# Optimization experiments

Measured on AMD Instinct MI355X. Metric: run time of the kernel, lower is better.

## Reference

```python
import jax, jax.numpy as jnp
import numpy as np

V = 200000      # num_symbols
E = 128         # embed_dim
PAD = V - 1     # padding index
KNN_K = 32
BQ, BS, NN, KT = 2048, 5, 128, 64
D = 2 * E       # d_model
STEPS = 4
H = 2 * D       # LSTMCell hidden


def setup_inputs():
    key = jax.random.key(0)
    ks = jax.random.split(key, 20)
    f = lambda k, s: jax.random.normal(k, s, dtype=jnp.float32) * 0.02
    emb = f(ks[0], (V, E)).at[PAD].set(0.0)  # padding row is zeros
    return dict(
        emb=emb,
        gcn_W=f(ks[1], (E, D)), gcn_wb=jnp.zeros((E,), jnp.float32),
        gate_W=f(ks[2], (1, D)), gate_b=jnp.zeros((1,), jnp.float32),
        se_w1=f(ks[3], (2 * D, D)), se_b1=jnp.zeros((2 * D,), jnp.float32),
        se_w2=f(ks[4], (D, 2 * D)), se_b2=jnp.zeros((D,), jnp.float32),
        ln_g=jnp.ones((D,), jnp.float32), ln_b=jnp.zeros((D,), jnp.float32),
        W_ih=f(ks[5], (4 * H, D)), W_hh=f(ks[6], (4 * H, H)),
        b_ih=jnp.zeros((4 * H,), jnp.float32), b_hh=jnp.zeros((4 * H,), jnp.float32),
        query=jax.random.randint(ks[7], (BQ, 2), 0, V),
        support=jax.random.randint(ks[8], (BS, 2), 0, V),
        q_l_conn=jax.random.randint(ks[9], (BQ, NN, 2), 0, V),
        q_l_deg=jax.random.randint(ks[10], (BQ,), 1, NN),
        q_r_conn=jax.random.randint(ks[11], (BQ, NN, 2), 0, V),
        q_r_deg=jax.random.randint(ks[12], (BQ,), 1, NN),
        s_l_conn=jax.random.randint(ks[13], (BS, NN, 2), 0, V),
        s_l_deg=jax.random.randint(ks[14], (BS,), 1, NN),
        s_r_conn=jax.random.randint(ks[15], (BS, NN, 2), 0, V),
        s_r_deg=jax.random.randint(ks[16], (BS,), 1, NN),
        knn_tab=jax.random.randint(ks[17], (V, KT), 0, V),
    )


def _cos(a, b):
    # F.cosine_similarity with eps=1e-8
    eps = 1e-8
    na = jnp.maximum(jnp.linalg.norm(a, axis=-1), eps)
    nb = jnp.maximum(jnp.linalg.norm(b, axis=-1), eps)
    return jnp.sum(a * b, axis=-1) / (na * nb)


def _neighbor_encoder(conn, eids, emb, gcn_W, gcn_wb, gate_W, gate_b, knn_tab):
    eids = jnp.where((eids < 0) | (eids >= V), PAD, eids)
    rel_e = emb[conn[..., 0]]            # [B,N,E]
    ent_e = emb[conn[..., 1]]            # [B,N,E]
    center = emb[eids][:, None, :]       # [B,1,E]
    # cosine-sim top-k neighbor selection
    sim = _cos(center, ent_e)            # [B,N]
    _, idx = jax.lax.top_k(sim, KNN_K)
    rel_k = jnp.take_along_axis(rel_e, idx[..., None], axis=1)
    ent_k = jnp.take_along_axis(ent_e, idx[..., None], axis=1)
    cat = jnp.concatenate([rel_k, ent_k], axis=-1)         # [B,k,2E]
    structural = jnp.tanh(jnp.mean(cat @ gcn_W.T + gcn_wb, axis=1))  # [B,E]
    # KNN-index branch
    kidx = knn_tab[eids]
    kidx = jnp.where((kidx < 0) | (kidx >= V), PAD, kidx)
    knn_e = emb[kidx]                    # [B,KT,E]
    sim2 = _cos(center, knn_e)
    _, idx2 = jax.lax.top_k(sim2, KNN_K)
    knn_k_e = jnp.take_along_axis(knn_e, idx2[..., None], axis=1)
    pad_rel = jnp.broadcast_to(emb[PAD], knn_k_e.shape)    # pad relation embedding
    cat2 = jnp.concatenate([pad_rel, knn_k_e], axis=-1)
    knn_mean = jnp.tanh(jnp.mean(cat2 @ gcn_W.T + gcn_wb, axis=1))
    # sigmoid gate fusing structural + knn representation
    gate_in = jnp.concatenate([structural, knn_mean], axis=-1)
    alpha = jax.nn.sigmoid(gate_in @ gate_W.T + gate_b)    # [B,1]
    return (1.0 - alpha) * structural + alpha * knn_mean


def _support_enc(x, w1, b1, w2, b2, g, b):
    h = jax.nn.relu(x @ w1.T + b1) @ w2.T + b2 + x
    mu = jnp.mean(h, axis=-1, keepdims=True)
    var = jnp.var(h, axis=-1, keepdims=True)
    return (h - mu) / jnp.sqrt(var + 1e-5) * g + b


def _query_enc(support, query, W_ih, W_hh, b_ih, b_hh):
    # GMatching LSTMCell matching network; support: [1,D], query: [B,D]
    B = query.shape[0]

    def step(carry, _):
        h_r, c = carry
        z = query @ W_ih.T + b_ih + h_r @ W_hh.T + b_hh
        i, f, g, o = jnp.split(z, 4, axis=-1)
        c2 = jax.nn.sigmoid(f) * c + jax.nn.sigmoid(i) * jnp.tanh(g)
        h2 = jax.nn.sigmoid(o) * jnp.tanh(c2)
        h = query + h2[:, :D]
        attn = jax.nn.softmax(h @ support.T, axis=1)       # [B,1]
        r = attn @ support                                  # [B,D]
        return (jnp.concatenate([h, r], axis=1), c2), h

    z0 = jnp.zeros((B, H), query.dtype)
    _, hs = jax.lax.scan(step, (z0, z0), None, length=STEPS)
    return hs[-1]


def reference(emb, gcn_W, gcn_wb, gate_W, gate_b, se_w1, se_b1, se_w2, se_b2,
              ln_g, ln_b, W_ih, W_hh, b_ih, b_hh,
              query, support, q_l_conn, q_l_deg, q_r_conn, q_r_deg,
              s_l_conn, s_l_deg, s_r_conn, s_r_deg, knn_tab):
    ne = lambda conn, eids: _neighbor_encoder(conn, eids, emb, gcn_W, gcn_wb,
                                              gate_W, gate_b, knn_tab)
    ql = ne(q_l_conn, query[:, 0])
    qr = ne(q_r_conn, query[:, 1])
    sl = ne(s_l_conn, support[:, 0])
    sr = ne(s_r_conn, support[:, 1])
    query_n = jnp.concatenate([ql, qr], axis=-1)   # [BQ,D]
    supp_n = jnp.concatenate([sl, sr], axis=-1)    # [BS,D]
    se = lambda x: _support_enc(x, se_w1, se_b1, se_w2, se_b2, ln_g, ln_b)
    support_g = jnp.mean(se(supp_n), axis=0, keepdims=True)   # [1,D]
    query_g = se(query_n)                                      # [BQ,D]
    query_f = _query_enc(support_g, query_g, W_ih, W_hh, b_ih, b_hh)
    qf = query_f / jnp.maximum(jnp.linalg.norm(query_f, axis=-1, keepdims=True), 1e-12)
    sg = support_g / jnp.maximum(jnp.linalg.norm(support_g, axis=-1, keepdims=True), 1e-12)
    return (qf @ sg.T).squeeze(-1)   # [BQ]
```

## Files before the change

### kernel.cpp

```cpp
#include <hip/hip_runtime.h>

#define Vn 200000
#define PADI 199999

typedef unsigned short ushort_t;
typedef unsigned int uint_t;
typedef __attribute__((ext_vector_type(8))) short short8;
typedef __attribute__((ext_vector_type(4))) float float4v;

__device__ __forceinline__ float sigm(float x) { return 1.f / (1.f + expf(-x)); }
__device__ __forceinline__ float dot4(float4 a, float4 b) {
  return a.x*b.x + a.y*b.y + a.z*b.z + a.w*b.w;
}
__device__ __forceinline__ ushort_t f2bf(float x) {
  uint_t u = __float_as_uint(x);
  uint_t r = (u + 0x7fffu + ((u >> 16) & 1u)) >> 16;
  return (ushort_t)r;
}
__device__ __forceinline__ float bf2f(ushort_t h) { return __uint_as_float(((uint_t)h) << 16); }

__device__ __forceinline__ float2 block_reduce2(float a, float b, float2* red) {
  #pragma unroll
  for (int off = 32; off; off >>= 1) { a += __shfl_down(a, off); b += __shfl_down(b, off); }
  __syncthreads();
  if ((threadIdx.x & 63) == 0) red[threadIdx.x >> 6] = make_float2(a, b);
  __syncthreads();
  float2 r;
  r.x = red[0].x + red[1].x + red[2].x + red[3].x;
  r.y = red[0].y + red[1].y + red[2].y + red[3].y;
  return r;
}

__global__ __launch_bounds__(256) void transpose_kernel(
    const float* __restrict__ in, float* __restrict__ out, int R, int Cfull, int c0, int Ct) {
  int idx = blockIdx.x * 256 + threadIdx.x;
  if (idx >= R * Ct) return;
  int c = idx / R, r = idx - c * R;
  out[idx] = in[(size_t)r * Cfull + c0 + c];
}

__global__ __launch_bounds__(256) void build_b2t_kernel(
    const float* __restrict__ W, ushort_t* __restrict__ b2t, int strideK) {
  int n = blockIdx.x, k = threadIdx.x;
  float v = W[(size_t)n*strideK + k];
  ushort_t hi = f2bf(v);
  ushort_t lo = f2bf(v - bf2f(hi));
  ushort_t* row = b2t + (size_t)n*768;
  row[k] = hi; row[256 + k] = hi; row[512 + k] = lo;
}

__global__ __launch_bounds__(256) void bias_sum_kernel(
    const float* __restrict__ a, const float* __restrict__ b, float* __restrict__ o) {
  int i = blockIdx.x*256 + threadIdx.x;
  o[i] = a[i] + b[i];
}

__global__ __launch_bounds__(256) void gemm_bf16_kernel(
    const ushort_t* __restrict__ A2, const ushort_t* __restrict__ B2T,
    float* __restrict__ C, const float* __restrict__ addmat,
    const float* __restrict__ cv, int ldc) {
  __shared__ ushort_t As[128*40];
  __shared__ ushort_t Bs[128*40];
  int t = threadIdx.x;
  int m0 = blockIdx.y * 128, n0 = blockIdx.x * 128;
  int wid = t >> 6, lane = t & 63;
  int wm = (wid >> 1) * 64, wn = (wid & 1) * 64;
  int q = lane >> 4, fr = lane & 15;
  float4v acc[4][4];
  #pragma unroll
  for (int i = 0; i < 4; ++i)
    #pragma unroll
    for (int j = 0; j < 4; ++j) acc[i][j] = (float4v)0.f;

  for (int k0 = 0; k0 < 768; k0 += 32) {
    #pragma unroll
    for (int rnd = 0; rnd < 2; ++rnd) {
      int idx = rnd*256 + t;
      int row = idx >> 2, ch = idx & 3;
      *(short8*)&As[row*40 + ch*8] = *(const short8*)(A2 + (size_t)(m0+row)*768 + k0 + ch*8);
      *(short8*)&Bs[row*40 + ch*8] = *(const short8*)(B2T + (size_t)(n0+row)*768 + k0 + ch*8);
    }
    __syncthreads();
    short8 af[4], bg[4];
    #pragma unroll
    for (int tm = 0; tm < 4; ++tm) af[tm] = *(const short8*)&As[(wm + tm*16 + fr)*40 + q*8];
    #pragma unroll
    for (int tn = 0; tn < 4; ++tn) bg[tn] = *(const short8*)&Bs[(wn + tn*16 + fr)*40 + q*8];
    #pragma unroll
    for (int tm = 0; tm < 4; ++tm)
      #pragma unroll
      for (int tn = 0; tn < 4; ++tn)
        acc[tm][tn] = __builtin_amdgcn_mfma_f32_16x16x32_bf16(af[tm], bg[tn], acc[tm][tn], 0, 0, 0);
    __syncthreads();
  }

  #pragma unroll
  for (int tm = 0; tm < 4; ++tm) {
    int gm = m0 + wm + tm*16 + q*4;
    #pragma unroll
    for (int tn = 0; tn < 4; ++tn) {
      int gn = n0 + wn + tn*16 + fr;
      float cvv = cv ? cv[gn] : 0.f;
      #pragma unroll
      for (int reg = 0; reg < 4; ++reg) {
        size_t off = (size_t)(gm + reg) * ldc + gn;
        float x = acc[tm][tn][reg] + cvv;
        if (addmat) x += addmat[off];
        C[off] = x;
      }
    }
  }
}

__global__ __launch_bounds__(256) void enc_kernel(
    const float* __restrict__ emb, const float* __restrict__ gcnW, const float* __restrict__ gcnb,
    const float* __restrict__ gateW, const float* __restrict__ gateb,
    const int* __restrict__ knn_tab,
    const int* __restrict__ query, const int* __restrict__ support,
    const int* __restrict__ qlc, const int* __restrict__ qrc,
    const int* __restrict__ slc, const int* __restrict__ src,
    float* __restrict__ xbuf) {
  __shared__ float center[128];
  __shared__ float sims[128];
  __shared__ float sims2[64];
  __shared__ int idr[128], ide[128];
  __shared__ int kidxs[64];
  __shared__ int sel[32], sel2[32];
  __shared__ int cnt1, cnt2;
  __shared__ float catbuf[256];
  __shared__ float knnA[128], knnB[128];
  __shared__ float part1[256], part2[256];
  __shared__ float structural[128], knnm[128];
  __shared__ float2 red2[4];

  int t = threadIdx.x;
  int g = blockIdx.x;
  int eid; const int* conn; float* outp;
  if (g < 2048)      { eid = query[2*g];                 conn = qlc + (size_t)g*256;      outp = xbuf + (size_t)g*256; }
  else if (g < 4096) { int b = g-2048; eid = query[2*b+1];  conn = qrc + (size_t)b*256;   outp = xbuf + (size_t)b*256 + 128; }
  else if (g < 4101) { int b = g-4096; eid = support[2*b];  conn = slc + (size_t)b*256;   outp = xbuf + (size_t)(2048+b)*256; }
  else               { int b = g-4101; eid = support[2*b+1]; conn = src + (size_t)b*256;  outp = xbuf + (size_t)(2048+b)*256 + 128; }
  if (eid < 0 || eid >= Vn) eid = PADI;

  if (t == 0) { cnt1 = 0; cnt2 = 0; }
  if (t < 128) {
    int2 cc = ((const int2*)conn)[t];
    idr[t] = cc.x; ide[t] = cc.y;
    center[t] = emb[(size_t)eid*128 + t];
  } else if (t < 192) {
    int kk = knn_tab[(size_t)eid*64 + (t-128)];
    kidxs[t-128] = (kk < 0 || kk >= Vn) ? PADI : kk;
  }
  __syncthreads();

  int gid = t >> 4, ll = t & 15;
  float4 cen0 = *(const float4*)&center[ll*8];
  float4 cen1 = *(const float4*)&center[ll*8 + 4];
  float cn2 = dot4(cen0, cen0) + dot4(cen1, cen1);
  #pragma unroll
  for (int off = 8; off; off >>= 1) cn2 += __shfl_down(cn2, off, 16);
  cn2 = __shfl(cn2, 0, 16);
  float cn = fmaxf(sqrtf(cn2), 1e-8f);

  #pragma unroll 2
  for (int it = 0; it < 4; ++it) {
    int n0 = it*32 + gid*2;
    int e0 = ide[n0], e1 = ide[n0+1];
    const float4* p0 = (const float4*)(emb + (size_t)e0*128);
    const float4* p1 = (const float4*)(emb + (size_t)e1*128);
    float4 a0 = p0[ll*2], b0 = p0[ll*2+1];
    float4 a1 = p1[ll*2], b1 = p1[ll*2+1];
    float d0 = dot4(a0, cen0) + dot4(b0, cen1), m0 = dot4(a0, a0) + dot4(b0, b0);
    float d1 = dot4(a1, cen0) + dot4(b1, cen1), m1 = dot4(a1, a1) + dot4(b1, b1);
    #pragma unroll
    for (int off = 8; off; off >>= 1) {
      d0 += __shfl_down(d0, off, 16); m0 += __shfl_down(m0, off, 16);
      d1 += __shfl_down(d1, off, 16); m1 += __shfl_down(m1, off, 16);
    }
    if (ll == 0) {
      sims[n0]   = d0 / (cn * fmaxf(sqrtf(m0), 1e-8f));
      sims[n0+1] = d1 / (cn * fmaxf(sqrtf(m1), 1e-8f));
    }
  }
  #pragma unroll 2
  for (int it = 0; it < 2; ++it) {
    int n0 = it*32 + gid*2;
    int e0 = kidxs[n0], e1 = kidxs[n0+1];
    const float4* p0 = (const float4*)(emb + (size_t)e0*128);
    const float4* p1 = (const float4*)(emb + (size_t)e1*128);
    float4 a0 = p0[ll*2], b0 = p0[ll*2+1];
    float4 a1 = p1[ll*2], b1 = p1[ll*2+1];
    float d0 = dot4(a0, cen0) + dot4(b0, cen1), m0 = dot4(a0, a0) + dot4(b0, b0);
    float d1 = dot4(a1, cen0) + dot4(b1, cen1), m1 = dot4(a1, a1) + dot4(b1, b1);
    #pragma unroll
    for (int off = 8; off; off >>= 1) {
      d0 += __shfl_down(d0, off, 16); m0 += __shfl_down(m0, off, 16);
      d1 += __shfl_down(d1, off, 16); m1 += __shfl_down(m1, off, 16);
    }
    if (ll == 0) {
      sims2[n0]   = d0 / (cn * fmaxf(sqrtf(m0), 1e-8f));
      sims2[n0+1] = d1 / (cn * fmaxf(sqrtf(m1), 1e-8f));
    }
  }
  __syncthreads();

  if (t < 128) {
    float my = sims[t];
    int c = 0;
    for (int j = 0; j < 128; ++j) {
      float sj = sims[j];
      c += (sj > my) || (sj == my && j < t);
    }
    if (c < 32) { int p = atomicAdd(&cnt1, 1); sel[p] = t; }
  } else if (t < 192) {
    int i = t - 128;
    float my = sims2[i];
    int c = 0;
    for (int j = 0; j < 64; ++j) {
      float sj = sims2[j];
      c += (sj > my) || (sj == my && j < i);
    }
    if (c < 32) { int p = atomicAdd(&cnt2, 1); sel2[p] = i; }
  }
  __syncthreads();

  {
    int i = t & 127;
    float a0 = 0.f, a1 = 0.f, a2 = 0.f, a3 = 0.f;
    float k0 = 0.f, k1 = 0.f;
    if (t < 128) {
      #pragma unroll 2
      for (int k = 0; k < 32; k += 4) {
        a0 += emb[(size_t)idr[sel[k+0]]*128 + i];
        a1 += emb[(size_t)idr[sel[k+1]]*128 + i];
        a2 += emb[(size_t)idr[sel[k+2]]*128 + i];
        a3 += emb[(size_t)idr[sel[k+3]]*128 + i];
      }
      catbuf[i] = (a0+a1+a2+a3) * (1.f/32.f);
      #pragma unroll 2
      for (int k = 0; k < 16; k += 2) {
        k0 += emb[(size_t)kidxs[sel2[k+0]]*128 + i];
        k1 += emb[(size_t)kidxs[sel2[k+1]]*128 + i];
      }
      knnA[i] = k0 + k1;
    } else {
      #pragma unroll 2
      for (int k = 0; k < 32; k += 4) {
        a0 += emb[(size_t)ide[sel[k+0]]*128 + i];
        a1 += emb[(size_t)ide[sel[k+1]]*128 + i];
        a2 += emb[(size_t)ide[sel[k+2]]*128 + i];
        a3 += emb[(size_t)ide[sel[k+3]]*128 + i];
      }
      catbuf[128 + i] = (a0+a1+a2+a3) * (1.f/32.f);
      #pragma unroll 2
      for (int k = 16; k < 32; k += 2) {
        k0 += emb[(size_t)kidxs[sel2[k+0]]*128 + i];
        k1 += emb[(size_t)kidxs[sel2[k+1]]*128 + i];
      }
      knnB[i] = k0 + k1;
    }
  }
  __syncthreads();

  {
    int i = t & 127, half = t >> 7;
    const float4* w1p = (const float4*)(gcnW + (size_t)i*256 + half*128);
    const float4* c1p = (const float4*)(catbuf + half*128);
    float p1 = 0.f;
    #pragma unroll 8
    for (int j = 0; j < 32; ++j) {
      float4 w = w1p[j], a = c1p[j];
      p1 += dot4(w, a);
    }
    const float4* w2p = (const float4*)(gcnW + (size_t)i*256 + 128 + half*64);
    const float4* kap = (const float4*)(knnA + half*64);
    const float4* kbp = (const float4*)(knnB + half*64);
    float p2 = 0.f;
    #pragma unroll 8
    for (int j = 0; j < 16; ++j) {
      float4 w = w2p[j], xa = kap[j], xb = kbp[j];
      float4 s = make_float4(xa.x+xb.x, xa.y+xb.y, xa.z+xb.z, xa.w+xb.w);
      p2 += dot4(w, s);
    }
    part1[t] = p1;
    part2[t] = p2 * (1.f/32.f);
  }
  __syncthreads();
  if (t < 128) {
    structural[t] = tanhf(part1[t] + part1[t+128] + gcnb[t]);
    knnm[t]       = tanhf(part2[t] + part2[t+128] + gcnb[t]);
  }
  __syncthreads();

  float gv = (t < 128) ? structural[t]*gateW[t] : knnm[t-128]*gateW[t];
  float2 rr = block_reduce2(gv, 0.f, red2);
  float alpha = sigm(rr.x + gateb[0]);
  if (t < 128) outp[t] = (1.f - alpha)*structural[t] + alpha*knnm[t];
}

__global__ __launch_bounds__(256) void qenc_kernel(
    const float* __restrict__ xin, const float* __restrict__ w1t, const float* __restrict__ b1,
    const float* __restrict__ w2t, const float* __restrict__ b2,
    const float* __restrict__ lng, const float* __restrict__ lnb,
    float* __restrict__ xout, ushort_t* __restrict__ a2) {
  __shared__ float xs[8][256];
  __shared__ float hsm[8][512];
  __shared__ float2 red2[4];
  int t = threadIdx.x;
  int r0 = blockIdx.x * 8;
  #pragma unroll
  for (int rr = 0; rr < 8; ++rr) xs[rr][t] = xin[(size_t)(r0+rr)*256 + t];
  __syncthreads();
  #pragma unroll
  for (int uo = 0; uo < 512; uo += 256) {
    int u = uo + t;
    float bv = b1[u];
    float acc[8];
    #pragma unroll
    for (int rr = 0; rr < 8; ++rr) acc[rr] = bv;
    for (int j4 = 0; j4 < 64; ++j4) {
      float w0 = w1t[(size_t)(j4*4+0)*512 + u];
      float w1v = w1t[(size_t)(j4*4+1)*512 + u];
      float w2v = w1t[(size_t)(j4*4+2)*512 + u];
      float w3 = w1t[(size_t)(j4*4+3)*512 + u];
      #pragma unroll
      for (int rr = 0; rr < 8; ++rr) {
        float4 x = *(const float4*)&xs[rr][j4*4];
        acc[rr] += x.x*w0 + x.y*w1v + x.z*w2v + x.w*w3;
      }
    }
    #pragma unroll
    for (int rr = 0; rr < 8; ++rr) hsm[rr][u] = fmaxf(acc[rr], 0.f);
  }
  __syncthreads();
  float val[8];
  {
    float bv = b2[t];
    #pragma unroll
    for (int rr = 0; rr < 8; ++rr) val[rr] = bv + xs[rr][t];
    for (int u4 = 0; u4 < 128; ++u4) {
      float w0 = w2t[(size_t)(u4*4+0)*256 + t];
      float w1v = w2t[(size_t)(u4*4+1)*256 + t];
      float w2v = w2t[(size_t)(u4*4+2)*256 + t];
      float w3 = w2t[(size_t)(u4*4+3)*256 + t];
      #pragma unroll
      for (int rr = 0; rr < 8; ++rr) {
        float4 h4 = *(const float4*)&hsm[rr][u4*4];
        val[rr] += h4.x*w0 + h4.y*w1v + h4.z*w2v + h4.w*w3;
      }
    }
  }
  float gv = lng[t], bv2 = lnb[t];
  for (int rr = 0; rr < 8; ++rr) {
    int r = r0 + rr;
    float2 sq = block_reduce2(val[rr], val[rr]*val[rr], red2);
    float mu  = sq.x * (1.f/256.f);
    float var = sq.y * (1.f/256.f) - mu*mu;
    float rs  = 1.f / sqrtf(var + 1e-5f);
    float ov  = (val[rr] - mu) * rs * gv + bv2;
    xout[(size_t)r*256 + t] = ov;
    if (r < 2048) {
      ushort_t hi = f2bf(ov);
      ushort_t lo = f2bf(ov - bf2f(hi));
      ushort_t* row = a2 + (size_t)r*768;
      row[t] = hi; row[256 + t] = lo; row[512 + t] = hi;
    }
  }
}

__global__ __launch_bounds__(256) void finalize_kernel(
    const float* __restrict__ qout, const float* __restrict__ whh,
    float* __restrict__ sg_hat, float* __restrict__ z_supp) {
  __shared__ float sg[256];
  __shared__ float2 red2[4];
  int t = threadIdx.x;
  float acc = 0.f;
  #pragma unroll
  for (int s = 0; s < 5; ++s) acc += qout[(size_t)(2048+s)*256 + t];
  float sgv = acc * 0.2f;
  sg[t] = sgv;
  float2 nn = block_reduce2(sgv*sgv, 0.f, red2);
  if (blockIdx.x == 0) sg_hat[t] = sgv / fmaxf(sqrtf(nn.x), 1e-12f);
  __syncthreads();
  int u = blockIdx.x*256 + t;
  const float4* w4 = (const float4*)(whh + (size_t)u*512 + 256);
  float a = 0.f;
  #pragma unroll 4
  for (int j4 = 0; j4 < 64; ++j4) {
    float4 wv = w4[j4];
    float4 sv = *(const float4*)&sg[j4*4];
    a += dot4(wv, sv);
  }
  z_supp[u] = a;
}

__global__ __launch_bounds__(256) void gate_kernel(
    const float* __restrict__ Z, const float* __restrict__ qg,
    float* __restrict__ c, ushort_t* __restrict__ a2, int step0) {
  int idx = blockIdx.x * 256 + threadIdx.x;
  int r = idx >> 9, j = idx & 511;
  const float* zr = Z + (size_t)r * 1792;
  float zi = zr[j], zf = zr[512 + j], zg = zr[1024 + j];
  float cold = step0 ? 0.f : c[idx];
  float c2 = sigm(zf) * cold + sigm(zi) * tanhf(zg);
  c[idx] = c2;
  if (j < 256) {
    float zo = zr[1536 + j];
    float h = qg[(size_t)r*256 + j] + sigm(zo) * tanhf(c2);
    ushort_t hi = f2bf(h);
    ushort_t lo = f2bf(h - bf2f(hi));
    ushort_t* row = a2 + (size_t)r*768;
    row[j] = hi; row[256 + j] = lo; row[512 + j] = hi;
  }
}

__global__ __launch_bounds__(256) void gatecos_kernel(
    const float* __restrict__ Z, const float* __restrict__ qg, const float* __restrict__ c,
    const float* __restrict__ sgh, float* __restrict__ out) {
  int wid = threadIdx.x >> 6, lane = threadIdx.x & 63;
  int r = blockIdx.x*4 + wid;
  const float* zr = Z + (size_t)r * 1792;
  float d = 0.f, n2 = 0.f;
  #pragma unroll
  for (int i = 0; i < 4; ++i) {
    int j = lane + i*64;
    float zi = zr[j], zf = zr[512 + j], zg = zr[1024 + j], zo = zr[1536 + j];
    float cold = c[(size_t)r*512 + j];
    float c2 = sigm(zf) * cold + sigm(zi) * tanhf(zg);
    float h = qg[(size_t)r*256 + j] + sigm(zo) * tanhf(c2);
    d += h * sgh[j];
    n2 += h * h;
  }
  #pragma unroll
  for (int off = 32; off; off >>= 1) { d += __shfl_down(d, off); n2 += __shfl_down(n2, off); }
  if (lane == 0) out[r] = d / fmaxf(sqrtf(n2), 1e-12f);
}

extern "C" void kernel_launch(void* const* d_in, const int* in_sizes, int n_in,
                              void* d_out, int out_size, void* d_ws, size_t ws_size,
                              hipStream_t stream) {
  const float* emb   = (const float*)d_in[0];
  const float* gcnW  = (const float*)d_in[1];
  const float* gcnb  = (const float*)d_in[2];
  const float* gateW = (const float*)d_in[3];
  const float* gateb = (const float*)d_in[4];
  const float* sew1  = (const float*)d_in[5];
  const float* seb1  = (const float*)d_in[6];
  const float* sew2  = (const float*)d_in[7];
  const float* seb2  = (const float*)d_in[8];
  const float* lng   = (const float*)d_in[9];
  const float* lnb   = (const float*)d_in[10];
  const float* Wih   = (const float*)d_in[11];
  const float* Whh   = (const float*)d_in[12];
  const float* bih   = (const float*)d_in[13];
  const float* bhh   = (const float*)d_in[14];
  const int* query   = (const int*)d_in[15];
  const int* support = (const int*)d_in[16];
  const int* qlc     = (const int*)d_in[17];
  const int* qrc     = (const int*)d_in[19];
  const int* slc     = (const int*)d_in[21];
  const int* src     = (const int*)d_in[23];
  const int* knn     = (const int*)d_in[25];
  float* out = (float*)d_out;

  float* w = (float*)d_ws;
  size_t o = 0;
  auto alloc = [&](size_t n) { float* p = w + o; o += (n + 15) & ~(size_t)15; return p; };
  float* xbuf      = alloc((size_t)2056*256);
  float* query_g   = alloc((size_t)2056*256);
  float* sg_hat    = alloc(256);
  float* z_supp    = alloc(1792);
  float* cbuf      = alloc((size_t)2048*512);
  float* Abuf      = alloc((size_t)2048*1792);
  float* Zbuf      = alloc((size_t)2048*1792);
  float* w1t       = alloc(256*512);
  float* w2t       = alloc(512*256);
  float* bias_s    = alloc(1792);
  ushort_t* A2     = (ushort_t*)alloc((size_t)2048*768/2);
  ushort_t* B2ih   = (ushort_t*)alloc((size_t)1792*768/2);
  ushort_t* B2hh   = (ushort_t*)alloc((size_t)1792*768/2);
  (void)ws_size; (void)in_sizes; (void)n_in; (void)out_size;

  transpose_kernel<<<512,  256, 0, stream>>>(sew1, w1t, 512, 256, 0, 256);
  transpose_kernel<<<1024, 256, 0, stream>>>(sew2, w2t, 256, 512, 0, 512);
  build_b2t_kernel<<<1792, 256, 0, stream>>>(Wih, B2ih, 256);
  build_b2t_kernel<<<1792, 256, 0, stream>>>(Whh, B2hh, 512);
  bias_sum_kernel<<<7, 256, 0, stream>>>(bih, bhh, bias_s);

  enc_kernel<<<4106, 256, 0, stream>>>(emb, gcnW, gcnb, gateW, gateb, knn,
                                       query, support, qlc, qrc, slc, src, xbuf);

  qenc_kernel<<<257, 256, 0, stream>>>(xbuf, w1t, seb1, w2t, seb2, lng, lnb, query_g, A2);

  finalize_kernel<<<7, 256, 0, stream>>>(query_g, Whh, sg_hat, z_supp);

  gemm_bf16_kernel<<<dim3(14,16), 256, 0, stream>>>(A2, B2ih, Abuf, nullptr, bias_s, 1792);
  gate_kernel<<<4096, 256, 0, stream>>>(Abuf, query_g, cbuf, A2, 1);
  for (int s = 1; s < 4; ++s) {
    gemm_bf16_kernel<<<dim3(14,16), 256, 0, stream>>>(A2, B2hh, Zbuf, Abuf, z_supp, 1792);
    if (s < 3) gate_kernel<<<4096, 256, 0, stream>>>(Zbuf, query_g, cbuf, A2, 0);
    else       gatecos_kernel<<<512, 256, 0, stream>>>(Zbuf, query_g, cbuf, sg_hat, out);
  }
}
```

Baseline: 581.8 us.

## Fuse LSTM pipeline into one persistent kernel with grid barriers

Merges the query-encoder, finalize, four GEMMs and gate kernels into a single persistent kernel of 448 blocks synchronized by atomic grid barriers. The five weight-prep kernels are merged into one launch, and the encoder's two similarity loops are unified into one pass that handles four rows at a time. The GEMM tile shrinks to 128x64 so the grid covers more blocks. The aim is to remove launch overhead and tail gaps between the many small kernels. In exchange it relies on all blocks being co-resident for the spin barrier, and the smaller GEMM tiles reuse less data.

Measured after the change: 998.9 us. 1.72x slower.

```diff
diff --git a/kernel.cpp b/kernel.cpp
--- a/kernel.cpp
+++ b/kernel.cpp
@@ -2,6 +2,7 @@
 
 #define Vn 200000
 #define PADI 199999
+#define NBLK 448
 
 typedef unsigned short ushort_t;
 typedef unsigned int uint_t;
@@ -31,84 +32,53 @@
   return r;
 }
 
-__global__ __launch_bounds__(256) void transpose_kernel(
-    const float* __restrict__ in, float* __restrict__ out, int R, int Cfull, int c0, int Ct) {
-  int idx = blockIdx.x * 256 + threadIdx.x;
-  if (idx >= R * Ct) return;
-  int c = idx / R, r = idx - c * R;
-  out[idx] = in[(size_t)r * Cfull + c0 + c];
-}
-
-__global__ __launch_bounds__(256) void build_b2t_kernel(
-    const float* __restrict__ W, ushort_t* __restrict__ b2t, int strideK) {
-  int n = blockIdx.x, k = threadIdx.x;
-  float v = W[(size_t)n*strideK + k];
-  ushort_t hi = f2bf(v);
-  ushort_t lo = f2bf(v - bf2f(hi));
-  ushort_t* row = b2t + (size_t)n*768;
-  row[k] = hi; row[256 + k] = hi; row[512 + k] = lo;
-}
-
-__global__ __launch_bounds__(256) void bias_sum_kernel(
-    const float* __restrict__ a, const float* __restrict__ b, float* __restrict__ o) {
-  int i = blockIdx.x*256 + threadIdx.x;
-  o[i] = a[i] + b[i];
-}
-
-__global__ __launch_bounds__(256) void gemm_bf16_kernel(
-    const ushort_t* __restrict__ A2, const ushort_t* __restrict__ B2T,
-    float* __restrict__ C, const float* __restrict__ addmat,
-    const float* __restrict__ cv, int ldc) {
-  __shared__ ushort_t As[128*40];
-  __shared__ ushort_t Bs[128*40];
-  int t = threadIdx.x;
-  int m0 = blockIdx.y * 128, n0 = blockIdx.x * 128;
-  int wid = t >> 6, lane = t & 63;
-  int wm = (wid >> 1) * 64, wn = (wid & 1) * 64;
-  int q = lane >> 4, fr = lane & 15;
-  float4v acc[4][4];
-  #pragma unroll
-  for (int i = 0; i < 4; ++i)
-    #pragma unroll
-    for (int j = 0; j < 4; ++j) acc[i][j] = (float4v)0.f;
-
-  for (int k0 = 0; k0 < 768; k0 += 32) {
-    #pragma unroll
-    for (int rnd = 0; rnd < 2; ++rnd) {
-      int idx = rnd*256 + t;
-      int row = idx >> 2, ch = idx & 3;
-      *(short8*)&As[row*40 + ch*8] = *(const short8*)(A2 + (size_t)(m0+row)*768 + k0 + ch*8);
-      *(short8*)&Bs[row*40 + ch*8] = *(const short8*)(B2T + (size_t)(n0+row)*768 + k0 + ch*8);
-    }
-    __syncthreads();
-    short8 af[4], bg[4];
-    #pragma unroll
-    for (int tm = 0; tm < 4; ++tm) af[tm] = *(const short8*)&As[(wm + tm*16 + fr)*40 + q*8];
-    #pragma unroll
-    for (int tn = 0; tn < 4; ++tn) bg[tn] = *(const short8*)&Bs[(wn + tn*16 + fr)*40 + q*8];
-    #pragma unroll
-    for (int tm = 0; tm < 4; ++tm)
-      #pragma unroll
-      for (int tn = 0; tn < 4; ++tn)
-        acc[tm][tn] = __builtin_amdgcn_mfma_f32_16x16x32_bf16(af[tm], bg[tn], acc[tm][tn], 0, 0, 0);
-    __syncthreads();
-  }
-
-  #pragma unroll
-  for (int tm = 0; tm < 4; ++tm) {
-    int gm = m0 + wm + tm*16 + q*4;
-    #pragma unroll
-    for (int tn = 0; tn < 4; ++tn) {
-      int gn = n0 + wn + tn*16 + fr;
-      float cvv = cv ? cv[gn] : 0.f;
-      #pragma unroll
-      for (int reg = 0; reg < 4; ++reg) {
-        size_t off = (size_t)(gm + reg) * ldc + gn;
-        float x = acc[tm][tn][reg] + cvv;
-        if (addmat) x += addmat[off];
-        C[off] = x;
-      }
-    }
+__device__ __forceinline__ void grid_bar(unsigned* cnt, int& phase) {
+  __syncthreads();
+  if (threadIdx.x == 0) {
+    phase++;
+    __threadfence();
+    __hip_atomic_fetch_add(cnt, 1u, __ATOMIC_RELEASE, __HIP_MEMORY_SCOPE_AGENT);
+    while (__hip_atomic_load(cnt, __ATOMIC_RELAXED, __HIP_MEMORY_SCOPE_AGENT) <
+           (unsigned)(NBLK * phase))
+      __builtin_amdgcn_s_sleep(2);
+    __threadfence();
+  }
+  __syncthreads();
+}
+
+__global__ __launch_bounds__(256) void prep_kernel(
+    const float* __restrict__ sew1, const float* __restrict__ sew2,
+    const float* __restrict__ Wih, const float* __restrict__ Whh,
+    const float* __restrict__ bih, const float* __restrict__ bhh,
+    float* __restrict__ w1t, float* __restrict__ w2t,
+    ushort_t* __restrict__ B2ih, ushort_t* __restrict__ B2hh,
+    float* __restrict__ bias_s, unsigned* __restrict__ bar) {
+  int b = blockIdx.x, t = threadIdx.x;
+  if (b < 512) {
+    int idx = b*256 + t;
+    int c = idx >> 9, r = idx & 511;
+    w1t[idx] = sew1[(size_t)r*256 + c];
+  } else if (b < 1024) {
+    int idx = (b-512)*256 + t;
+    int c = idx >> 8, r = idx & 255;
+    w2t[idx] = sew2[(size_t)r*512 + c];
+  } else if (b < 2816) {
+    int n = b - 1024;
+    float v = Wih[(size_t)n*256 + t];
+    ushort_t hi = f2bf(v), lo = f2bf(v - bf2f(hi));
+    ushort_t* row = B2ih + (size_t)n*768;
+    row[t] = hi; row[256+t] = hi; row[512+t] = lo;
+  } else if (b < 4608) {
+    int n = b - 2816;
+    float v = Whh[(size_t)n*512 + t];
+    ushort_t hi = f2bf(v), lo = f2bf(v - bf2f(hi));
+    ushort_t* row = B2hh + (size_t)n*768;
+    row[t] = hi; row[256+t] = hi; row[512+t] = lo;
+  } else if (b < 4615) {
+    int i = (b-4608)*256 + t;
+    bias_s[i] = bih[i] + bhh[i];
+  } else {
+    if (t < 8) bar[t] = 0u;
   }
 }
 
@@ -121,8 +91,7 @@
     const int* __restrict__ slc, const int* __restrict__ src,
     float* __restrict__ xbuf) {
   __shared__ float center[128];
-  __shared__ float sims[128];
-  __shared__ float sims2[64];
+  __shared__ float simsu[192];
   __shared__ int idr[128], ide[128];
   __shared__ int kidxs[64];
   __shared__ int sel[32], sel2[32];
@@ -162,62 +131,53 @@
   cn2 = __shfl(cn2, 0, 16);
   float cn = fmaxf(sqrtf(cn2), 1e-8f);
 
-  #pragma unroll 2
-  for (int it = 0; it < 4; ++it) {
-    int n0 = it*32 + gid*2;
-    int e0 = ide[n0], e1 = ide[n0+1];
-    const float4* p0 = (const float4*)(emb + (size_t)e0*128);
-    const float4* p1 = (const float4*)(emb + (size_t)e1*128);
-    float4 a0 = p0[ll*2], b0 = p0[ll*2+1];
-    float4 a1 = p1[ll*2], b1 = p1[ll*2+1];
-    float d0 = dot4(a0, cen0) + dot4(b0, cen1), m0 = dot4(a0, a0) + dot4(b0, b0);
-    float d1 = dot4(a1, cen0) + dot4(b1, cen1), m1 = dot4(a1, a1) + dot4(b1, b1);
+  #pragma unroll
+  for (int it = 0; it < 3; ++it) {
+    int rbase = it*64 + gid*4;
+    int e[4];
+    #pragma unroll
+    for (int rr = 0; rr < 4; ++rr) {
+      int n = rbase + rr;
+      e[rr] = (n < 128) ? ide[n] : kidxs[n-128];
+    }
+    float d[4], m[4];
+    #pragma unroll
+    for (int rr = 0; rr < 4; ++rr) {
+      const float4* p = (const float4*)(emb + (size_t)e[rr]*128);
+      float4 a = p[ll*2], bb = p[ll*2+1];
+      d[rr] = dot4(a, cen0) + dot4(bb, cen1);
+      m[rr] = dot4(a, a) + dot4(bb, bb);
+    }
     #pragma unroll
     for (int off = 8; off; off >>= 1) {
-      d0 += __shfl_down(d0, off, 16); m0 += __shfl_down(m0, off, 16);
-      d1 += __shfl_down(d1, off, 16); m1 += __shfl_down(m1, off, 16);
+      #pragma unroll
+      for (int rr = 0; rr < 4; ++rr) {
+        d[rr] += __shfl_down(d[rr], off, 16);
+        m[rr] += __shfl_down(m[rr], off, 16);
+      }
     }
     if (ll == 0) {
-      sims[n0]   = d0 / (cn * fmaxf(sqrtf(m0), 1e-8f));
-      sims[n0+1] = d1 / (cn * fmaxf(sqrtf(m1), 1e-8f));
-    }
-  }
-  #pragma unroll 2
-  for (int it = 0; it < 2; ++it) {
-    int n0 = it*32 + gid*2;
-    int e0 = kidxs[n0], e1 = kidxs[n0+1];
-    const float4* p0 = (const float4*)(emb + (size_t)e0*128);
-    const float4* p1 = (const float4*)(emb + (size_t)e1*128);
-    float4 a0 = p0[ll*2], b0 = p0[ll*2+1];
-    float4 a1 = p1[ll*2], b1 = p1[ll*2+1];
-    float d0 = dot4(a0, cen0) + dot4(b0, cen1), m0 = dot4(a0, a0) + dot4(b0, b0);
-    float d1 = dot4(a1, cen0) + dot4(b1, cen1), m1 = dot4(a1, a1) + dot4(b1, b1);
-    #pragma unroll
-    for (int off = 8; off; off >>= 1) {
-      d0 += __shfl_down(d0, off, 16); m0 += __shfl_down(m0, off, 16);
-      d1 += __shfl_down(d1, off, 16); m1 += __shfl_down(m1, off, 16);
-    }
-    if (ll == 0) {
-      sims2[n0]   = d0 / (cn * fmaxf(sqrtf(m0), 1e-8f));
-      sims2[n0+1] = d1 / (cn * fmaxf(sqrtf(m1), 1e-8f));
+      #pragma unroll
+      for (int rr = 0; rr < 4; ++rr)
+        simsu[rbase+rr] = d[rr] / (cn * fmaxf(sqrtf(m[rr]), 1e-8f));
     }
   }
   __syncthreads();
 
   if (t < 128) {
-    float my = sims[t];
+    float my = simsu[t];
     int c = 0;
     for (int j = 0; j < 128; ++j) {
-      float sj = sims[j];
+      float sj = simsu[j];
       c += (sj > my) || (sj == my && j < t);
     }
     if (c < 32) { int p = atomicAdd(&cnt1, 1); sel[p] = t; }
   } else if (t < 192) {
     int i = t - 128;
-    float my = sims2[i];
+    float my = simsu[128 + i];
     int c = 0;
     for (int j = 0; j < 64; ++j) {
-      float sj = sims2[j];
+      float sj = simsu[128 + j];
       c += (sj > my) || (sj == my && j < i);
     }
     if (c < 32) { int p = atomicAdd(&cnt2, 1); sel2[p] = i; }
@@ -298,142 +258,220 @@
   if (t < 128) outp[t] = (1.f - alpha)*structural[t] + alpha*knnm[t];
 }
 
-__global__ __launch_bounds__(256) void qenc_kernel(
-    const float* __restrict__ xin, const float* __restrict__ w1t, const float* __restrict__ b1,
+__device__ __forceinline__ void gemm_phase(
+    const ushort_t* __restrict__ A2, const ushort_t* __restrict__ B2T,
+    float* __restrict__ C, const float* __restrict__ addmat, const float* __restrict__ cv,
+    int bx, int by, int t, char* smem) {
+  ushort_t* As = (ushort_t*)smem;
+  ushort_t* Bs = (ushort_t*)(smem + 10240);
+  int m0 = by*128, n0 = bx*64;
+  int wid = t >> 6, lane = t & 63;
+  int wm = (wid >> 1) * 64, wn = (wid & 1) * 32;
+  int q = lane >> 4, fr = lane & 15;
+  float4v acc[4][2];
+  #pragma unroll
+  for (int i = 0; i < 4; ++i) { acc[i][0] = (float4v)0.f; acc[i][1] = (float4v)0.f; }
+
+  int row = t >> 2, ch = t & 3;
+  for (int k0 = 0; k0 < 768; k0 += 32) {
+    *(short8*)&As[row*40 + ch*8]      = *(const short8*)(A2 + (size_t)(m0+row)*768 + k0 + ch*8);
+    *(short8*)&As[(row+64)*40 + ch*8] = *(const short8*)(A2 + (size_t)(m0+row+64)*768 + k0 + ch*8);
+    *(short8*)&Bs[row*40 + ch*8]      = *(const short8*)(B2T + (size_t)(n0+row)*768 + k0 + ch*8);
+    __syncthreads();
+    short8 af[4], bg[2];
+    #pragma unroll
+    for (int mt = 0; mt < 4; ++mt) af[mt] = *(const short8*)&As[(wm + mt*16 + fr)*40 + q*8];
+    #pragma unroll
+    for (int nt = 0; nt < 2; ++nt) bg[nt] = *(const short8*)&Bs[(wn + nt*16 + fr)*40 + q*8];
+    #pragma unroll
+    for (int mt = 0; mt < 4; ++mt)
+      #pragma unroll
+      for (int nt = 0; nt < 2; ++nt)
+        acc[mt][nt] = __builtin_amdgcn_mfma_f32_16x16x32_bf16(af[mt], bg[nt], acc[mt][nt], 0, 0, 0);
+    __syncthreads();
+  }
+  #pragma unroll
+  for (int mt = 0; mt < 4; ++mt) {
+    int gm = m0 + wm + mt*16 + q*4;
+    #pragma unroll
+    for (int nt = 0; nt < 2; ++nt) {
+      int gn = n0 + wn + nt*16 + fr;
+      float cvv = cv ? cv[gn] : 0.f;
+      #pragma unroll
+      for (int reg = 0; reg < 4; ++reg) {
+        size_t off = (size_t)(gm + reg) * 1792 + gn;
+        float x = acc[mt][nt][reg] + cvv;
+        if (addmat) x += addmat[off];
+        C[off] = x;
+      }
+    }
+  }
+}
+
+__device__ __forceinline__ void gate_phase(
+    const float* __restrict__ Z, const float* __restrict__ qg,
+    float* __restrict__ c, ushort_t* __restrict__ a2, int step0, int b, int t) {
+  for (int idx = b*256 + t; idx < 2048*512; idx += NBLK*256) {
+    int r = idx >> 9, j = idx & 511;
+    const float* zr = Z + (size_t)r * 1792;
+    float zi = zr[j], zf = zr[512 + j], zg = zr[1024 + j];
+    float cold = step0 ? 0.f : c[idx];
+    float c2 = sigm(zf) * cold + sigm(zi) * tanhf(zg);
+    c[idx] = c2;
+    if (j < 256) {
+      float zo = zr[1536 + j];
+      float h = qg[(size_t)r*256 + j] + sigm(zo) * tanhf(c2);
+      ushort_t hi = f2bf(h), lo = f2bf(h - bf2f(hi));
+      ushort_t* row = a2 + (size_t)r*768;
+      row[j] = hi; row[256 + j] = lo; row[512 + j] = hi;
+    }
+  }
+}
+
+__global__ __launch_bounds__(256, 2) void lstm_kernel(
+    const float* __restrict__ xbuf, const float* __restrict__ w1t, const float* __restrict__ b1,
     const float* __restrict__ w2t, const float* __restrict__ b2,
     const float* __restrict__ lng, const float* __restrict__ lnb,
-    float* __restrict__ xout, ushort_t* __restrict__ a2) {
-  __shared__ float xs[8][256];
-  __shared__ float hsm[8][512];
-  __shared__ float2 red2[4];
+    const float* __restrict__ whh_full,
+    const ushort_t* __restrict__ B2ih, const ushort_t* __restrict__ B2hh,
+    const float* __restrict__ bias_s,
+    float* __restrict__ qg, ushort_t* __restrict__ A2,
+    float* __restrict__ z_supp, float* __restrict__ sg_hat,
+    float* __restrict__ Abuf, float* __restrict__ Zbuf, float* __restrict__ cbuf,
+    float* __restrict__ outv, unsigned* __restrict__ bar) {
+  __shared__ __align__(16) char smem[24640];
   int t = threadIdx.x;
-  int r0 = blockIdx.x * 8;
-  #pragma unroll
-  for (int rr = 0; rr < 8; ++rr) xs[rr][t] = xin[(size_t)(r0+rr)*256 + t];
-  __syncthreads();
-  #pragma unroll
-  for (int uo = 0; uo < 512; uo += 256) {
-    int u = uo + t;
-    float bv = b1[u];
-    float acc[8];
-    #pragma unroll
-    for (int rr = 0; rr < 8; ++rr) acc[rr] = bv;
+  int b = blockIdx.x;
+  int phase = 0;
+
+  if (b < 257) {
+    float (*xs)[256]  = (float (*)[256])smem;
+    float (*hsm)[512] = (float (*)[512])(smem + 8192);
+    float2* red2 = (float2*)(smem + 8192 + 16384);
+    int r0 = b * 8;
+    #pragma unroll
+    for (int rr = 0; rr < 8; ++rr) xs[rr][t] = xbuf[(size_t)(r0+rr)*256 + t];
+    __syncthreads();
+    #pragma unroll
+    for (int uo = 0; uo < 512; uo += 256) {
+      int u = uo + t;
+      float bv = b1[u];
+      float acc[8];
+      #pragma unroll
+      for (int rr = 0; rr < 8; ++rr) acc[rr] = bv;
+      for (int j4 = 0; j4 < 64; ++j4) {
+        float w0 = w1t[(size_t)(j4*4+0)*512 + u];
+        float w1v = w1t[(size_t)(j4*4+1)*512 + u];
+        float w2v = w1t[(size_t)(j4*4+2)*512 + u];
+        float w3 = w1t[(size_t)(j4*4+3)*512 + u];
+        #pragma unroll
+        for (int rr = 0; rr < 8; ++rr) {
+          float4 x = *(const float4*)&xs[rr][j4*4];
+          acc[rr] += x.x*w0 + x.y*w1v + x.z*w2v + x.w*w3;
+        }
+      }
+      #pragma unroll
+      for (int rr = 0; rr < 8; ++rr) hsm[rr][u] = fmaxf(acc[rr], 0.f);
+    }
+    __syncthreads();
+    float val[8];
+    {
+      float bv = b2[t];
+      #pragma unroll
+      for (int rr = 0; rr < 8; ++rr) val[rr] = bv + xs[rr][t];
+      for (int u4 = 0; u4 < 128; ++u4) {
+        float w0 = w2t[(size_t)(u4*4+0)*256 + t];
+        float w1v = w2t[(size_t)(u4*4+1)*256 + t];
+        float w2v = w2t[(size_t)(u4*4+2)*256 + t];
+        float w3 = w2t[(size_t)(u4*4+3)*256 + t];
+        #pragma unroll
+        for (int rr = 0; rr < 8; ++rr) {
+          float4 h4 = *(const float4*)&hsm[rr][u4*4];
+          val[rr] += h4.x*w0 + h4.y*w1v + h4.z*w2v + h4.w*w3;
+        }
+      }
+    }
+    float gvv = lng[t], bv2 = lnb[t];
+    for (int rr = 0; rr < 8; ++rr) {
+      int r = r0 + rr;
+      float2 sq = block_reduce2(val[rr], val[rr]*val[rr], red2);
+      float mu  = sq.x * (1.f/256.f);
+      float var = sq.y * (1.f/256.f) - mu*mu;
+      float rs  = 1.f / sqrtf(var + 1e-5f);
+      float ov  = (val[rr] - mu) * rs * gvv + bv2;
+      qg[(size_t)r*256 + t] = ov;
+      if (r < 2048) {
+        ushort_t hi = f2bf(ov), lo = f2bf(ov - bf2f(hi));
+        ushort_t* row = A2 + (size_t)r*768;
+        row[t] = hi; row[256 + t] = lo; row[512 + t] = hi;
+      }
+    }
+  }
+  grid_bar(bar, phase);
+
+  if (b < 7) {
+    float* sg = (float*)smem;
+    float2* red2 = (float2*)(smem + 1024);
+    float acc = 0.f;
+    #pragma unroll
+    for (int s = 0; s < 5; ++s) acc += qg[(size_t)(2048+s)*256 + t];
+    float sgv = acc * 0.2f;
+    sg[t] = sgv;
+    float2 nn = block_reduce2(sgv*sgv, 0.f, red2);
+    if (b == 0) sg_hat[t] = sgv / fmaxf(sqrtf(nn.x), 1e-12f);
+    __syncthreads();
+    int u = b*256 + t;
+    const float4* w4 = (const float4*)(whh_full + (size_t)u*512 + 256);
+    float a = 0.f;
+    #pragma unroll 4
     for (int j4 = 0; j4 < 64; ++j4) {
-      float w0 = w1t[(size_t)(j4*4+0)*512 + u];
-      float w1v = w1t[(size_t)(j4*4+1)*512 + u];
-      float w2v = w1t[(size_t)(j4*4+2)*512 + u];
-      float w3 = w1t[(size_t)(j4*4+3)*512 + u];
-      #pragma unroll
-      for (int rr = 0; rr < 8; ++rr) {
-        float4 x = *(const float4*)&xs[rr][j4*4];
-        acc[rr] += x.x*w0 + x.y*w1v + x.z*w2v + x.w*w3;
-      }
-    }
-    #pragma unroll
-    for (int rr = 0; rr < 8; ++rr) hsm[rr][u] = fmaxf(acc[rr], 0.f);
-  }
-  __syncthreads();
-  float val[8];
-  {
-    float bv = b2[t];
-    #pragma unroll
-    for (int rr = 0; rr < 8; ++rr) val[rr] = bv + xs[rr][t];
-    for (int u4 = 0; u4 < 128; ++u4) {
-      float w0 = w2t[(size_t)(u4*4+0)*256 + t];
-      float w1v = w2t[(size_t)(u4*4+1)*256 + t];
-      float w2v = w2t[(size_t)(u4*4+2)*256 + t];
-      float w3 = w2t[(size_t)(u4*4+3)*256 + t];
-      #pragma unroll
-      for (int rr = 0; rr < 8; ++rr) {
-        float4 h4 = *(const float4*)&hsm[rr][u4*4];
-        val[rr] += h4.x*w0 + h4.y*w1v + h4.z*w2v + h4.w*w3;
-      }
-    }
-  }
-  float gv = lng[t], bv2 = lnb[t];
-  for (int rr = 0; rr < 8; ++rr) {
-    int r = r0 + rr;
-    float2 sq = block_reduce2(val[rr], val[rr]*val[rr], red2);
-    float mu  = sq.x * (1.f/256.f);
-    float var = sq.y * (1.f/256.f) - mu*mu;
-    float rs  = 1.f / sqrtf(var + 1e-5f);
-    float ov  = (val[rr] - mu) * rs * gv + bv2;
-    xout[(size_t)r*256 + t] = ov;
-    if (r < 2048) {
-      ushort_t hi = f2bf(ov);
-      ushort_t lo = f2bf(ov - bf2f(hi));
-      ushort_t* row = a2 + (size_t)r*768;
-      row[t] = hi; row[256 + t] = lo; row[512 + t] = hi;
-    }
-  }
-}
-
-__global__ __launch_bounds__(256) void finalize_kernel(
-    const float* __restrict__ qout, const float* __restrict__ whh,
-    float* __restrict__ sg_hat, float* __restrict__ z_supp) {
-  __shared__ float sg[256];
-  __shared__ float2 red2[4];
-  int t = threadIdx.x;
-  float acc = 0.f;
-  #pragma unroll
-  for (int s = 0; s < 5; ++s) acc += qout[(size_t)(2048+s)*256 + t];
-  float sgv = acc * 0.2f;
-  sg[t] = sgv;
-  float2 nn = block_reduce2(sgv*sgv, 0.f, red2);
-  if (blockIdx.x == 0) sg_hat[t] = sgv / fmaxf(sqrtf(nn.x), 1e-12f);
-  __syncthreads();
-  int u = blockIdx.x*256 + t;
-  const float4* w4 = (const float4*)(whh + (size_t)u*512 + 256);
-  float a = 0.f;
-  #pragma unroll 4
-  for (int j4 = 0; j4 < 64; ++j4) {
-    float4 wv = w4[j4];
-    float4 sv = *(const float4*)&sg[j4*4];
-    a += dot4(wv, sv);
-  }
-  z_supp[u] = a;
-}
-
-__global__ __launch_bounds__(256) void gate_kernel(
-    const float* __restrict__ Z, const float* __restrict__ qg,
-    float* __restrict__ c, ushort_t* __restrict__ a2, int step0) {
-  int idx = blockIdx.x * 256 + threadIdx.x;
-  int r = idx >> 9, j = idx & 511;
-  const float* zr = Z + (size_t)r * 1792;
-  float zi = zr[j], zf = zr[512 + j], zg = zr[1024 + j];
-  float cold = step0 ? 0.f : c[idx];
-  float c2 = sigm(zf) * cold + sigm(zi) * tanhf(zg);
-  c[idx] = c2;
-  if (j < 256) {
-    float zo = zr[1536 + j];
-    float h = qg[(size_t)r*256 + j] + sigm(zo) * tanhf(c2);
-    ushort_t hi = f2bf(h);
-    ushort_t lo = f2bf(h - bf2f(hi));
-    ushort_t* row = a2 + (size_t)r*768;
-    row[j] = hi; row[256 + j] = lo; row[512 + j] = hi;
-  }
-}
-
-__global__ __launch_bounds__(256) void gatecos_kernel(
-    const float* __restrict__ Z, const float* __restrict__ qg, const float* __restrict__ c,
-    const float* __restrict__ sgh, float* __restrict__ out) {
-  int wid = threadIdx.x >> 6, lane = threadIdx.x & 63;
-  int r = blockIdx.x*4 + wid;
-  const float* zr = Z + (size_t)r * 1792;
-  float d = 0.f, n2 = 0.f;
-  #pragma unroll
-  for (int i = 0; i < 4; ++i) {
-    int j = lane + i*64;
-    float zi = zr[j], zf = zr[512 + j], zg = zr[1024 + j], zo = zr[1536 + j];
-    float cold = c[(size_t)r*512 + j];
-    float c2 = sigm(zf) * cold + sigm(zi) * tanhf(zg);
-    float h = qg[(size_t)r*256 + j] + sigm(zo) * tanhf(c2);
-    d += h * sgh[j];
-    n2 += h * h;
-  }
-  #pragma unroll
-  for (int off = 32; off; off >>= 1) { d += __shfl_down(d, off); n2 += __shfl_down(n2, off); }
-  if (lane == 0) out[r] = d / fmaxf(sqrtf(n2), 1e-12f);
+      float4 wv = w4[j4];
+      float4 sv = *(const float4*)&sg[j4*4];
+      a += dot4(wv, sv);
+    }
+    z_supp[u] = a;
+    __syncthreads();
+  }
+
+  gemm_phase(A2, B2ih, Abuf, nullptr, bias_s, b % 28, b / 28, t, smem);
+  grid_bar(bar, phase);
+
+  gate_phase(Abuf, qg, cbuf, A2, 1, b, t);
+  grid_bar(bar, phase);
+
+  for (int s = 1; s <= 3; ++s) {
+    if (s < 3) {
+      gemm_phase(A2, B2hh, Zbuf, Abuf, z_supp, b % 28, b / 28, t, smem);
+    } else if (b < 256) {
+      int bxi = b & 15, by = b >> 4;
+      int bx = (bxi >> 2) * 8 + (bxi & 3);
+      gemm_phase(A2, B2hh, Zbuf, Abuf, z_supp, bx, by, t, smem);
+    }
+    grid_bar(bar, phase);
+    if (s < 3) {
+      gate_phase(Zbuf, qg, cbuf, A2, 0, b, t);
+      grid_bar(bar, phase);
+    } else {
+      int wid = t >> 6, lane = t & 63;
+      for (int r = b*4 + wid; r < 2048; r += NBLK*4) {
+        const float* zr = Zbuf + (size_t)r * 1792;
+        float d = 0.f, n2 = 0.f;
+        #pragma unroll
+        for (int i = 0; i < 4; ++i) {
+          int j = lane + i*64;
+          float zi = zr[j], zf = zr[512 + j], zg = zr[1024 + j], zo = zr[1536 + j];
+          float cold = cbuf[(size_t)r*512 + j];
+          float c2 = sigm(zf) * cold + sigm(zi) * tanhf(zg);
+          float h = qg[(size_t)r*256 + j] + sigm(zo) * tanhf(c2);
+          d += h * sg_hat[j];
+          n2 += h * h;
+        }
+        #pragma unroll
+        for (int off = 32; off; off >>= 1) { d += __shfl_down(d, off); n2 += __shfl_down(n2, off); }
+        if (lane == 0) outv[r] = d / fmaxf(sqrtf(n2), 1e-12f);
+      }
+    }
+  }
 }
 
 extern "C" void kernel_launch(void* const* d_in, const int* in_sizes, int n_in,
@@ -476,29 +514,20 @@
   float* w1t       = alloc(256*512);
   float* w2t       = alloc(512*256);
   float* bias_s    = alloc(1792);
+  unsigned* bar    = (unsigned*)alloc(16);
   ushort_t* A2     = (ushort_t*)alloc((size_t)2048*768/2);
   ushort_t* B2ih   = (ushort_t*)alloc((size_t)1792*768/2);
   ushort_t* B2hh   = (ushort_t*)alloc((size_t)1792*768/2);
   (void)ws_size; (void)in_sizes; (void)n_in; (void)out_size;
 
-  transpose_kernel<<<512,  256, 0, stream>>>(sew1, w1t, 512, 256, 0, 256);
-  transpose_kernel<<<1024, 256, 0, stream>>>(sew2, w2t, 256, 512, 0, 512);
-  build_b2t_kernel<<<1792, 256, 0, stream>>>(Wih, B2ih, 256);
-  build_b2t_kernel<<<1792, 256, 0, stream>>>(Whh, B2hh, 512);
-  bias_sum_kernel<<<7, 256, 0, stream>>>(bih, bhh, bias_s);
+  prep_kernel<<<4616, 256, 0, stream>>>(sew1, sew2, Wih, Whh, bih, bhh,
+                                        w1t, w2t, B2ih, B2hh, bias_s, bar);
 
   enc_kernel<<<4106, 256, 0, stream>>>(emb, gcnW, gcnb, gateW, gateb, knn,
                                        query, support, qlc, qrc, slc, src, xbuf);
 
-  qenc_kernel<<<257, 256, 0, stream>>>(xbuf, w1t, seb1, w2t, seb2, lng, lnb, query_g, A2);
-
-  finalize_kernel<<<7, 256, 0, stream>>>(query_g, Whh, sg_hat, z_supp);
-
-  gemm_bf16_kernel<<<dim3(14,16), 256, 0, stream>>>(A2, B2ih, Abuf, nullptr, bias_s, 1792);
-  gate_kernel<<<4096, 256, 0, stream>>>(Abuf, query_g, cbuf, A2, 1);
-  for (int s = 1; s < 4; ++s) {
-    gemm_bf16_kernel<<<dim3(14,16), 256, 0, stream>>>(A2, B2hh, Zbuf, Abuf, z_supp, 1792);
-    if (s < 3) gate_kernel<<<4096, 256, 0, stream>>>(Zbuf, query_g, cbuf, A2, 0);
-    else       gatecos_kernel<<<512, 256, 0, stream>>>(Zbuf, query_g, cbuf, sg_hat, out);
-  }
-}
+  lstm_kernel<<<NBLK, 256, 0, stream>>>(xbuf, w1t, seb1, w2t, seb2, lng, lnb, Whh,
+                                        B2ih, B2hh, bias_s,
+                                        query_g, A2, z_supp, sg_hat,
+                                        Abuf, Zbuf, cbuf, out, bar);
+}
```
